# Optimization experiments

Hardware: AMD Instinct MI355X
Metric: run time of the kernel (lower is better)

The kernel has to match this reference:

```python
import jax, jax.numpy as jnp
import numpy as np
import math

DIM = 768
FFN_DIM = 4 * DIM
EPS = 1e-5

def layer_norm(x, gamma, beta):
    mu = jnp.mean(x, axis=-1, keepdims=True)
    var = jnp.var(x, axis=-1, keepdims=True)
    return (x - mu) * jax.lax.rsqrt(var + EPS) * gamma + beta

def setup_inputs() -> dict:
    key = jax.random.key(0)
    ks = jax.random.split(key, 8)
    b, n, d = 8, 2048, DIM
    s = 1.0 / math.sqrt(d)
    x = jax.random.normal(ks[0], (b, n, d), dtype=jnp.float32)
    Wq = jax.random.normal(ks[1], (d, d), dtype=jnp.float32) * s
    Wk = jax.random.normal(ks[2], (d, d), dtype=jnp.float32) * s
    Wv = jax.random.normal(ks[3], (d, d), dtype=jnp.float32) * s
    W1 = jax.random.normal(ks[4], (d, FFN_DIM), dtype=jnp.float32) * s
    b1 = jnp.zeros((FFN_DIM,), dtype=jnp.float32)
    W2 = jax.random.normal(ks[5], (FFN_DIM, d), dtype=jnp.float32) * (1.0 / math.sqrt(FFN_DIM))
    b2 = jnp.zeros((d,), dtype=jnp.float32)
    g1 = jnp.ones((d,), dtype=jnp.float32); be1 = jnp.zeros((d,), dtype=jnp.float32)
    g2 = jnp.ones((d,), dtype=jnp.float32); be2 = jnp.zeros((d,), dtype=jnp.float32)
    return {"x": x, "Wq": Wq, "Wk": Wk, "Wv": Wv, "ln1_g": g1, "ln1_b": be1,
            "W1": W1, "b1": b1, "W2": W2, "b2": b2, "ln2_g": g2, "ln2_b": be2}

def reference(x, Wq, Wk, Wv, ln1_g, ln1_b, W1, b1, W2, b2, ln2_g, ln2_b):
    # Self-attention (single head, full dim; dropout in eval mode => identity)
    Q = jnp.einsum('bnd,de->bne', x, Wq)
    K = jnp.einsum('bnd,de->bne', x, Wk)
    V = jnp.einsum('bnd,de->bne', x, Wv)
    scores = jnp.einsum('bnd,bmd->bnm', Q, K) / math.sqrt(DIM)  # [b,n,n]
    attn = jax.nn.softmax(scores, axis=-1)
    O = jnp.einsum('bnm,bmd->bnd', attn, V)
    h = layer_norm(x + O, ln1_g, ln1_b)
    # FFN with exact GELU (torch nn.GELU default)
    hidden = jax.nn.gelu(jnp.einsum('bnd,df->bnf', h, W1) + b1, approximate=False)
    out = jnp.einsum('bnf,fd->bnd', hidden, W2) + b2
    return layer_norm(h + out, ln2_g, ln2_b)
```

## Files before the change

### kernel.cpp

```cpp
#include <hip/hip_runtime.h>
#include <hip/hip_bf16.h>
#include <math.h>

using u16 = unsigned short;
typedef __bf16 bf16x8 __attribute__((ext_vector_type(8)));
typedef float f32x4 __attribute__((ext_vector_type(4)));
typedef u16 u16x8 __attribute__((ext_vector_type(8)));

__device__ __forceinline__ u16 f2b(float f) {
  union { float f; unsigned u; } c; c.f = f;
  unsigned r = c.u + 0x7fffu + ((c.u >> 16) & 1u);
  return (u16)(r >> 16);
}
__device__ __forceinline__ float b2f(u16 h) {
  union { unsigned u; float f; } c; c.u = ((unsigned)h) << 16;
  return c.f;
}

__device__ __forceinline__ float fast_gelu(float t) {
  float y = fminf(1.5957691216f * t + 0.07135481283f * t * t * t, 80.f);
  float e = __expf(y);
  return t * e * (1.0f / (e + 1.0f));
}

#define EPI_BF16 0
#define EPI_BF16_SCALE 1
#define EPI_GELU_BIAS 2
#define EPI_F32_BIAS 3
#define EPI_BF16_BIAS 4

#define GLDS16(src, dst)                                                     \
  __builtin_amdgcn_global_load_lds(                                          \
      (const __attribute__((address_space(1))) void*)(src),                  \
      (__attribute__((address_space(3))) void*)(dst), 16, 0, 0)

__device__ __forceinline__ int xswz(int o, int n) {
  int q = n >> 3, r = n & 7, x = o & 7, i = o >> 3;
  return (x < r ? x * (q + 1) : r * (q + 1) + (x - r) * q) + i;
}

template <int EPI>
__device__ __forceinline__ void epi_store(
    void* Cg, const float* bias, float v, long long off, int ccol, float scale)
{
  if (EPI == EPI_BF16) {
    ((u16*)Cg)[off] = f2b(v);
  } else if (EPI == EPI_BF16_SCALE) {
    ((u16*)Cg)[off] = f2b(v * scale);
  } else if (EPI == EPI_GELU_BIAS) {
    ((u16*)Cg)[off] = f2b(fast_gelu(v + bias[ccol]));
  } else if (EPI == EPI_F32_BIAS) {
    ((float*)Cg)[off] = v + bias[ccol];
  } else {
    ((u16*)Cg)[off] = f2b(v + bias[ccol]);
  }
}

template <int EPI>
__global__ __launch_bounds__(512, 2) void gemm256(
    const u16* __restrict__ Ag, const u16* __restrict__ Bg,
    void* __restrict__ Cg, const float* __restrict__ bias,
    int nbx, int K, float scale, int lda, int ldb, int ldc,
    long long sAz, long long sBz, long long sCz)
{
  __shared__ __align__(16) u16 lds[65536];

  const int tid = threadIdx.x;
  const int wave = tid >> 6, lane = tid & 63;
  const int wr = wave >> 2, wc = wave & 3;
  const int id = xswz(blockIdx.x, gridDim.x);
  const int bx = id % nbx, by = id / nbx;
  const int m0 = by * 256, n0 = bx * 256;
  const long long z = blockIdx.z;
  const u16* A = Ag + z * sAz + (long long)m0 * lda;
  const u16* B = Bg + z * sBz + (long long)n0 * ldb;

  const int rA = wave * 32 + (lane >> 2);
  const int slot = (lane & 3) ^ ((rA >> 1) & 3);
  const u16* a0 = A + (long long)rA * lda + slot * 8;
  const u16* a1 = a0 + (long long)16 * lda;
  const u16* b0 = B + (long long)rA * ldb + slot * 8;
  const u16* b1 = b0 + (long long)16 * ldb;
  const int d0 = wave * 32 * 32;
  const int d1 = (wave * 32 + 16) * 32;

  int offA[8], offB[4];
#pragma unroll
  for (int mf = 0; mf < 8; ++mf) {
    int r = wr * 128 + mf * 16 + (lane & 15);
    int b = r * 64 + ((lane >> 4) << 4);
    offA[mf] = b ^ (((b >> 7) & 3) << 4);
  }
#pragma unroll
  for (int nf = 0; nf < 4; ++nf) {
    int r = wc * 64 + nf * 16 + (lane & 15);
    int b = r * 64 + ((lane >> 4) << 4);
    offB[nf] = b ^ (((b >> 7) & 3) << 4);
  }

  f32x4 acc[8][4];
#pragma unroll
  for (int m = 0; m < 8; ++m)
#pragma unroll
    for (int n = 0; n < 4; ++n) acc[m][n] = f32x4{0.f, 0.f, 0.f, 0.f};

  const char* ldsc = (const char*)lds;
  const int NT = K >> 6;

  GLDS16(a0, lds + 0 * 8192 + d0);  GLDS16(a1, lds + 0 * 8192 + d1);
  GLDS16(b0, lds + 2 * 8192 + d0);  GLDS16(b1, lds + 2 * 8192 + d1);
  GLDS16(a0 + 32, lds + 1 * 8192 + d0);  GLDS16(a1 + 32, lds + 1 * 8192 + d1);
  GLDS16(b0 + 32, lds + 3 * 8192 + d0);  GLDS16(b1 + 32, lds + 3 * 8192 + d1);
  asm volatile("s_waitcnt vmcnt(4)" ::: "memory");
  asm volatile("s_barrier" ::: "memory");

  for (int t = 0; t < NT; ++t) {
    const int buf = t & 1, nb = buf ^ 1;
    const int kc = (t + 1 < NT) ? ((t + 1) << 6) : 0;
    const char* pA0 = ldsc + (buf * 4 + 0) * 16384;
    const char* pA1 = ldsc + (buf * 4 + 1) * 16384;
    const char* pB0 = ldsc + (buf * 4 + 2) * 16384;
    const char* pB1 = ldsc + (buf * 4 + 3) * 16384;
    u16* q = lds + nb * 4 * 8192;

    bf16x8 Af[4], Bf[4];

    GLDS16(a0 + kc, q + 0 * 8192 + d0);  GLDS16(a1 + kc, q + 0 * 8192 + d1);
    GLDS16(b0 + kc, q + 2 * 8192 + d0);  GLDS16(b1 + kc, q + 2 * 8192 + d1);
#pragma unroll
    for (int m = 0; m < 4; ++m) Af[m] = *(const bf16x8*)(pA0 + offA[m]);
#pragma unroll
    for (int n = 0; n < 4; ++n) Bf[n] = *(const bf16x8*)(pB0 + offB[n]);
    __builtin_amdgcn_s_setprio(1);
#pragma unroll
    for (int m = 0; m < 4; ++m)
#pragma unroll
      for (int n = 0; n < 4; ++n)
        acc[m][n] = __builtin_amdgcn_mfma_f32_16x16x32_bf16(Af[m], Bf[n], acc[m][n], 0, 0, 0);
    __builtin_amdgcn_s_setprio(0);

    GLDS16(a0 + kc + 32, q + 1 * 8192 + d0);  GLDS16(a1 + kc + 32, q + 1 * 8192 + d1);
    GLDS16(b0 + kc + 32, q + 3 * 8192 + d0);  GLDS16(b1 + kc + 32, q + 3 * 8192 + d1);
#pragma unroll
    for (int m = 0; m < 4; ++m) Af[m] = *(const bf16x8*)(pA0 + offA[4 + m]);
    __builtin_amdgcn_s_setprio(1);
#pragma unroll
    for (int m = 0; m < 4; ++m)
#pragma unroll
      for (int n = 0; n < 4; ++n)
        acc[4 + m][n] = __builtin_amdgcn_mfma_f32_16x16x32_bf16(Af[m], Bf[n], acc[4 + m][n], 0, 0, 0);
    __builtin_amdgcn_s_setprio(0);
    asm volatile("s_waitcnt vmcnt(8)" ::: "memory");
    asm volatile("s_barrier" ::: "memory");

#pragma unroll
    for (int m = 0; m < 4; ++m) Af[m] = *(const bf16x8*)(pA1 + offA[m]);
#pragma unroll
    for (int n = 0; n < 4; ++n) Bf[n] = *(const bf16x8*)(pB1 + offB[n]);
    __builtin_amdgcn_s_setprio(1);
#pragma unroll
    for (int m = 0; m < 4; ++m)
#pragma unroll
      for (int n = 0; n < 4; ++n)
        acc[m][n] = __builtin_amdgcn_mfma_f32_16x16x32_bf16(Af[m], Bf[n], acc[m][n], 0, 0, 0);
    __builtin_amdgcn_s_setprio(0);

#pragma unroll
    for (int m = 0; m < 4; ++m) Af[m] = *(const bf16x8*)(pA1 + offA[4 + m]);
    __builtin_amdgcn_s_setprio(1);
#pragma unroll
    for (int m = 0; m < 4; ++m)
#pragma unroll
      for (int n = 0; n < 4; ++n)
        acc[4 + m][n] = __builtin_amdgcn_mfma_f32_16x16x32_bf16(Af[m], Bf[n], acc[4 + m][n], 0, 0, 0);
    __builtin_amdgcn_s_setprio(0);
    asm volatile("s_waitcnt vmcnt(4)" ::: "memory");
    asm volatile("s_barrier" ::: "memory");
  }

#pragma unroll
  for (int mf = 0; mf < 8; ++mf) {
#pragma unroll
    for (int nf = 0; nf < 4; ++nf) {
      const int crow = m0 + wr * 128 + mf * 16 + (lane >> 4) * 4;
      const int ccol = n0 + wc * 64 + nf * 16 + (lane & 15);
#pragma unroll
      for (int j = 0; j < 4; ++j) {
        const long long off = (long long)(crow + j) * ldc + ccol + z * sCz;
        epi_store<EPI>(Cg, bias, acc[mf][nf][j], off, ccol, scale);
      }
    }
  }
}

template <int EPI>
__global__ __launch_bounds__(256, 2) void gemm128(
    const u16* __restrict__ Ag, const u16* __restrict__ Bg,
    void* __restrict__ Cg, const float* __restrict__ bias,
    int nbx, int K, float scale, int lda, int ldb, int ldc,
    long long sAz, long long sBz, long long sCz)
{
  __shared__ __align__(16) u16 lds[32768];

  const int tid = threadIdx.x;
  const int wave = tid >> 6, lane = tid & 63;
  const int wr = wave >> 1, wc = wave & 1;
  const int id = xswz(blockIdx.x, gridDim.x);
  const int bx = id % nbx, by = id / nbx;
  const int m0 = by * 128, n0 = bx * 128;
  const long long z = blockIdx.z;
  const u16* A = Ag + z * sAz + (long long)m0 * lda;
  const u16* B = Bg + z * sBz + (long long)n0 * ldb;

  const int rA = wave * 32 + (lane >> 2);
  const int slot = (lane & 3) ^ ((rA >> 1) & 3);
  const u16* a0 = A + (long long)rA * lda + slot * 8;
  const u16* a1 = a0 + (long long)16 * lda;
  const u16* b0 = B + (long long)rA * ldb + slot * 8;
  const u16* b1 = b0 + (long long)16 * ldb;
  const int d0 = wave * 32 * 32;
  const int d1 = (wave * 32 + 16) * 32;

  int offA[4], offB[4];
#pragma unroll
  for (int f = 0; f < 4; ++f) {
    int ra = wr * 64 + f * 16 + (lane & 15);
    int ba = ra * 64 + ((lane >> 4) << 4);
    offA[f] = ba ^ (((ba >> 7) & 3) << 4);
    int rb = wc * 64 + f * 16 + (lane & 15);
    int bb = rb * 64 + ((lane >> 4) << 4);
    offB[f] = bb ^ (((bb >> 7) & 3) << 4);
  }

  f32x4 acc[4][4];
#pragma unroll
  for (int m = 0; m < 4; ++m)
#pragma unroll
    for (int n = 0; n < 4; ++n) acc[m][n] = f32x4{0.f, 0.f, 0.f, 0.f};

  const char* ldsc = (const char*)lds;
  const int NT = K >> 6;

  GLDS16(a0, lds + 0 * 4096 + d0);  GLDS16(a1, lds + 0 * 4096 + d1);
  GLDS16(b0, lds + 2 * 4096 + d0);  GLDS16(b1, lds + 2 * 4096 + d1);
  GLDS16(a0 + 32, lds + 1 * 4096 + d0);  GLDS16(a1 + 32, lds + 1 * 4096 + d1);
  GLDS16(b0 + 32, lds + 3 * 4096 + d0);  GLDS16(b1 + 32, lds + 3 * 4096 + d1);
  asm volatile("s_waitcnt vmcnt(4)" ::: "memory");
  asm volatile("s_barrier" ::: "memory");

  for (int t = 0; t < NT; ++t) {
    const int buf = t & 1, nb = buf ^ 1;
    const int kc = (t + 1 < NT) ? ((t + 1) << 6) : 0;
    const char* pA0 = ldsc + (buf * 4 + 0) * 8192;
    const char* pA1 = ldsc + (buf * 4 + 1) * 8192;
    const char* pB0 = ldsc + (buf * 4 + 2) * 8192;
    const char* pB1 = ldsc + (buf * 4 + 3) * 8192;
    u16* q = lds + nb * 4 * 4096;

    bf16x8 Af[4], Bf[4];

    GLDS16(a0 + kc, q + 0 * 4096 + d0);  GLDS16(a1 + kc, q + 0 * 4096 + d1);
    GLDS16(b0 + kc, q + 2 * 4096 + d0);  GLDS16(b1 + kc, q + 2 * 4096 + d1);
#pragma unroll
    for (int m = 0; m < 4; ++m) Af[m] = *(const bf16x8*)(pA0 + offA[m]);
#pragma unroll
    for (int n = 0; n < 4; ++n) Bf[n] = *(const bf16x8*)(pB0 + offB[n]);
    __builtin_amdgcn_s_setprio(1);
#pragma unroll
    for (int m = 0; m < 4; ++m)
#pragma unroll
      for (int n = 0; n < 4; ++n)
        acc[m][n] = __builtin_amdgcn_mfma_f32_16x16x32_bf16(Af[m], Bf[n], acc[m][n], 0, 0, 0);
    __builtin_amdgcn_s_setprio(0);
    asm volatile("s_waitcnt vmcnt(4)" ::: "memory");
    asm volatile("s_barrier" ::: "memory");

    GLDS16(a0 + kc + 32, q + 1 * 4096 + d0);  GLDS16(a1 + kc + 32, q + 1 * 4096 + d1);
    GLDS16(b0 + kc + 32, q + 3 * 4096 + d0);  GLDS16(b1 + kc + 32, q + 3 * 4096 + d1);
#pragma unroll
    for (int m = 0; m < 4; ++m) Af[m] = *(const bf16x8*)(pA1 + offA[m]);
#pragma unroll
    for (int n = 0; n < 4; ++n) Bf[n] = *(const bf16x8*)(pB1 + offB[n]);
    __builtin_amdgcn_s_setprio(1);
#pragma unroll
    for (int m = 0; m < 4; ++m)
#pragma unroll
      for (int n = 0; n < 4; ++n)
        acc[m][n] = __builtin_amdgcn_mfma_f32_16x16x32_bf16(Af[m], Bf[n], acc[m][n], 0, 0, 0);
    __builtin_amdgcn_s_setprio(0);
    asm volatile("s_waitcnt vmcnt(4)" ::: "memory");
    asm volatile("s_barrier" ::: "memory");
  }

#pragma unroll
  for (int mf = 0; mf < 4; ++mf) {
#pragma unroll
    for (int nf = 0; nf < 4; ++nf) {
      const int crow = m0 + wr * 64 + mf * 16 + (lane >> 4) * 4;
      const int ccol = n0 + wc * 64 + nf * 16 + (lane & 15);
#pragma unroll
      for (int j = 0; j < 4; ++j) {
        const long long off = (long long)(crow + j) * ldc + ccol + z * sCz;
        epi_store<EPI>(Cg, bias, acc[mf][nf][j], off, ccol, scale);
      }
    }
  }
}

__global__ __launch_bounds__(256) void cast_f32_bf16(
    const float* __restrict__ x, u16* __restrict__ y, long long n4)
{
  const long long i = (long long)blockIdx.x * 256 + threadIdx.x;
  if (i >= n4) return;
  const float4 v = ((const float4*)x)[i];
  ushort4 o;
  o.x = f2b(v.x); o.y = f2b(v.y); o.z = f2b(v.z); o.w = f2b(v.w);
  ((ushort4*)y)[i] = o;
}

template <bool SRC_BF16>
__global__ __launch_bounds__(256) void transpose_cast(
    const void* __restrict__ srcv, u16* __restrict__ dst, int R, int C, int ldsrc,
    long long szSrc, long long szDst)
{
  __shared__ float tile[32][33];
  const long long zs = (long long)blockIdx.z * szSrc;
  const long long zd = (long long)blockIdx.z * szDst;
  const int c0 = blockIdx.x * 32, r0 = blockIdx.y * 32;
  const int tx = threadIdx.x & 31, ty = threadIdx.x >> 5;
#pragma unroll
  for (int i = 0; i < 4; ++i) {
    const int r = r0 + ty + i * 8;
    float v;
    if (SRC_BF16) v = b2f(((const u16*)srcv)[zs + (long long)r * ldsrc + c0 + tx]);
    else          v = ((const float*)srcv)[zs + (long long)r * ldsrc + c0 + tx];
    tile[ty + i * 8][tx] = v;
  }
  __syncthreads();
#pragma unroll
  for (int i = 0; i < 4; ++i) {
    const int c = c0 + ty + i * 8;
    dst[zd + (long long)c * R + r0 + tx] = f2b(tile[tx][ty + i * 8]);
  }
}

__global__ __launch_bounds__(256) void softmax_rows(
    u16* __restrict__ S, int ncol)
{
  __shared__ float red[8];
  const long long row = blockIdx.x;
  u16* s = S + row * ncol;
  const int t = threadIdx.x;

  const u16x8 u = *(const u16x8*)&s[t * 8];
  float v[8];
#pragma unroll
  for (int j = 0; j < 8; ++j) v[j] = b2f(u[j]);

  float mx = v[0];
#pragma unroll
  for (int j = 1; j < 8; ++j) mx = fmaxf(mx, v[j]);
  for (int o = 32; o; o >>= 1) mx = fmaxf(mx, __shfl_xor(mx, o));
  if ((t & 63) == 0) red[t >> 6] = mx;
  __syncthreads();
  mx = fmaxf(fmaxf(red[0], red[1]), fmaxf(red[2], red[3]));

  float sum = 0.f;
#pragma unroll
  for (int j = 0; j < 8; ++j) { v[j] = __expf(v[j] - mx); sum += v[j]; }
  for (int o = 32; o; o >>= 1) sum += __shfl_xor(sum, o);
  if ((t & 63) == 0) red[4 + (t >> 6)] = sum;
  __syncthreads();
  sum = red[4] + red[5] + red[6] + red[7];

  const float inv = 1.0f / sum;
  u16x8 o8;
#pragma unroll
  for (int j = 0; j < 8; ++j) o8[j] = f2b(v[j] * inv);
  *(u16x8*)&s[t * 8] = o8;
}

__global__ __launch_bounds__(256) void ln1_kernel(
    const float* __restrict__ x, const u16* __restrict__ O,
    const float* __restrict__ g, const float* __restrict__ be,
    u16* __restrict__ h)
{
  __shared__ float red[8];
  const long long row = blockIdx.x;
  const float* xr = x + row * 768;
  const u16* orow = O + row * 768;
  const int t = threadIdx.x, base = t * 3;

  float v[3];
#pragma unroll
  for (int j = 0; j < 3; ++j) v[j] = xr[base + j] + b2f(orow[base + j]);
  float s = v[0] + v[1] + v[2];
  float ss = v[0] * v[0] + v[1] * v[1] + v[2] * v[2];
  for (int o = 32; o; o >>= 1) { s += __shfl_xor(s, o); ss += __shfl_xor(ss, o); }
  if ((t & 63) == 0) { red[t >> 6] = s; red[4 + (t >> 6)] = ss; }
  __syncthreads();
  s = red[0] + red[1] + red[2] + red[3];
  ss = red[4] + red[5] + red[6] + red[7];
  const float mu = s * (1.0f / 768.0f);
  const float var = ss * (1.0f / 768.0f) - mu * mu;
  const float inv = rsqrtf(var + 1e-5f);
#pragma unroll
  for (int j = 0; j < 3; ++j) {
    const float o = (v[j] - mu) * inv * g[base + j] + be[base + j];
    h[row * 768 + base + j] = f2b(o);
  }
}

__global__ __launch_bounds__(256) void ln2_kernel(
    const u16* __restrict__ h, const u16* __restrict__ ob,
    const float* __restrict__ g, const float* __restrict__ be,
    float* __restrict__ y)
{
  __shared__ float red[8];
  const long long row = blockIdx.x;
  const u16* hr = h + row * 768;
  const u16* orow = ob + row * 768;
  const int t = threadIdx.x, base = t * 3;

  float v[3];
#pragma unroll
  for (int j = 0; j < 3; ++j) v[j] = b2f(hr[base + j]) + b2f(orow[base + j]);
  float s = v[0] + v[1] + v[2];
  float ss = v[0] * v[0] + v[1] * v[1] + v[2] * v[2];
  for (int o = 32; o; o >>= 1) { s += __shfl_xor(s, o); ss += __shfl_xor(ss, o); }
  if ((t & 63) == 0) { red[t >> 6] = s; red[4 + (t >> 6)] = ss; }
  __syncthreads();
  s = red[0] + red[1] + red[2] + red[3];
  ss = red[4] + red[5] + red[6] + red[7];
  const float mu = s * (1.0f / 768.0f);
  const float var = ss * (1.0f / 768.0f) - mu * mu;
  const float inv = rsqrtf(var + 1e-5f);
#pragma unroll
  for (int j = 0; j < 3; ++j) {
    y[row * 768 + base + j] = (v[j] - mu) * inv * g[base + j] + be[base + j];
  }
}

extern "C" void kernel_launch(void* const* d_in, const int* in_sizes, int n_in,
                              void* d_out, int out_size, void* d_ws, size_t ws_size,
                              hipStream_t stream)
{
  const int Bb = 8, Nn = 2048, D = 768, F = 3072, E = 1536;
  const int M = Bb * Nn;
  const long long MD = (long long)M * D;

  const float* x   = (const float*)d_in[0];
  const float* Wq  = (const float*)d_in[1];
  const float* Wk  = (const float*)d_in[2];
  const float* Wv  = (const float*)d_in[3];
  const float* g1  = (const float*)d_in[4];
  const float* be1 = (const float*)d_in[5];
  const float* W1  = (const float*)d_in[6];
  const float* b1  = (const float*)d_in[7];
  const float* W2  = (const float*)d_in[8];
  const float* b2  = (const float*)d_in[9];
  const float* g2  = (const float*)d_in[10];
  const float* be2 = (const float*)d_in[11];

  u16* xb   = (u16*)d_out;
  u16* wqkt = xb + MD;
  u16* wvt  = wqkt + (size_t)E * D;

  char* w = (char*)d_ws;
  size_t off = 0;
  auto alloc = [&](size_t bytes) { void* p = w + off; off += bytes; return p; };
  u16* w1t = (u16*)alloc((size_t)F * D * 2);
  u16* w2t = (u16*)alloc((size_t)D * F * 2);
  u16* hb  = (u16*)alloc((size_t)MD * 2);
  u16* qk  = (u16*)alloc((size_t)M * E * 2);
  u16* Vt  = (u16*)alloc((size_t)Bb * D * Nn * 2);
  u16* S   = (u16*)alloc((size_t)Bb * Nn * Nn * 2);
  u16* O   = (u16*)alloc((size_t)MD * 2);
  u16* hidden = qk;
  u16* outf   = qk + (size_t)M * F;

  const dim3 tcb(256);
  const float scl = 0.03608439182435161f;

  cast_f32_bf16<<<(unsigned)(MD / 4 / 256), 256, 0, stream>>>(x, xb, MD / 4);
  transpose_cast<false><<<dim3(D / 32, D / 32, 1), tcb, 0, stream>>>(Wq, wqkt, D, D, D, 0, 0);
  transpose_cast<false><<<dim3(D / 32, D / 32, 1), tcb, 0, stream>>>(Wk, wqkt + D * D, D, D, D, 0, 0);
  transpose_cast<false><<<dim3(D / 32, D / 32, 1), tcb, 0, stream>>>(Wv, wvt, D, D, D, 0, 0);
  transpose_cast<false><<<dim3(F / 32, D / 32, 1), tcb, 0, stream>>>(W1, w1t, D, F, F, 0, 0);
  transpose_cast<false><<<dim3(D / 32, F / 32, 1), tcb, 0, stream>>>(W2, w2t, F, D, D, 0, 0);

  gemm256<EPI_BF16><<<dim3(6 * 64, 1, 1), 512, 0, stream>>>(
      xb, wqkt, qk, nullptr, 6, D, 1.f, D, D, E, 0, 0, 0);

  gemm128<EPI_BF16><<<dim3(16 * 6, 1, Bb), 256, 0, stream>>>(
      wvt, xb, Vt, nullptr, 16, D, 1.f, D, D, Nn,
      0, (long long)Nn * D, (long long)D * Nn);

  gemm256<EPI_BF16_SCALE><<<dim3(8 * 8, 1, Bb), 512, 0, stream>>>(
      qk, qk + D, S, nullptr, 8, D, scl, E, E, Nn,
      (long long)Nn * E, (long long)Nn * E, (long long)Nn * Nn);

  softmax_rows<<<M, 256, 0, stream>>>(S, Nn);

  gemm128<EPI_BF16><<<dim3(6 * 16, 1, Bb), 256, 0, stream>>>(
      S, Vt, O, nullptr, 6, Nn, 1.f, Nn, Nn, D,
      (long long)Nn * Nn, (long long)D * Nn, (long long)Nn * D);

  ln1_kernel<<<M, 256, 0, stream>>>(x, O, g1, be1, hb);

  gemm256<EPI_GELU_BIAS><<<dim3(12 * 64, 1, 1), 512, 0, stream>>>(
      hb, w1t, hidden, b1, 12, D, 1.f, D, D, F, 0, 0, 0);

  gemm128<EPI_BF16_BIAS><<<dim3(6 * 128, 1, 1), 256, 0, stream>>>(
      hidden, w2t, outf, b2, 6, F, 1.f, F, F, D, 0, 0, 0);

  ln2_kernel<<<M, 256, 0, stream>>>(hb, outf, g2, be2, (float*)d_out);
}
```

Baseline: 501.1 us.

## Fuse softmax exp and row-sum into QK^T GEMM epilogue, defer normalization to LN1

Removes the separate softmax kernel. The QK^T GEMM epilogue now writes exp(score) without subtracting the row max, clamped at 60, and atomically accumulates per-row sums into a zeroed float buffer. LN1 divides the unnormalized PV output by that sum. This saves a full read and write pass over the large score matrix, at the cost of skipping max subtraction (overflow or precision risk for large scores), atomics, and an extra zeroing kernel. The gemm256 main loop is also reordered to interleave the A and B tile loads with extra barriers, and gemm128 gets extra barriers too.

After: 488.2 us. 1.03x faster.

```diff
diff --git a/kernel.cpp b/kernel.cpp
--- a/kernel.cpp
+++ b/kernel.cpp
@@ -24,9 +24,8 @@
 }
 
 #define EPI_BF16 0
-#define EPI_BF16_SCALE 1
+#define EPI_EXP_SUM 1
 #define EPI_GELU_BIAS 2
-#define EPI_F32_BIAS 3
 #define EPI_BF16_BIAS 4
 
 #define GLDS16(src, dst)                                                     \
@@ -45,12 +44,8 @@
 {
   if (EPI == EPI_BF16) {
     ((u16*)Cg)[off] = f2b(v);
-  } else if (EPI == EPI_BF16_SCALE) {
-    ((u16*)Cg)[off] = f2b(v * scale);
   } else if (EPI == EPI_GELU_BIAS) {
     ((u16*)Cg)[off] = f2b(fast_gelu(v + bias[ccol]));
-  } else if (EPI == EPI_F32_BIAS) {
-    ((float*)Cg)[off] = v + bias[ccol];
   } else {
     ((u16*)Cg)[off] = f2b(v + bias[ccol]);
   }
@@ -61,7 +56,8 @@
     const u16* __restrict__ Ag, const u16* __restrict__ Bg,
     void* __restrict__ Cg, const float* __restrict__ bias,
     int nbx, int K, float scale, int lda, int ldb, int ldc,
-    long long sAz, long long sBz, long long sCz)
+    long long sAz, long long sBz, long long sCz,
+    float* __restrict__ lsum, int lzs)
 {
   __shared__ __align__(16) u16 lds[65536];
 
@@ -125,12 +121,13 @@
 
     bf16x8 Af[4], Bf[4];
 
-    GLDS16(a0 + kc, q + 0 * 8192 + d0);  GLDS16(a1 + kc, q + 0 * 8192 + d1);
-    GLDS16(b0 + kc, q + 2 * 8192 + d0);  GLDS16(b1 + kc, q + 2 * 8192 + d1);
+    GLDS16(a0 + kc, q + 0 * 8192 + d0);
+    GLDS16(a1 + kc, q + 0 * 8192 + d1);
 #pragma unroll
     for (int m = 0; m < 4; ++m) Af[m] = *(const bf16x8*)(pA0 + offA[m]);
 #pragma unroll
     for (int n = 0; n < 4; ++n) Bf[n] = *(const bf16x8*)(pB0 + offB[n]);
+    asm volatile("s_barrier" ::: "memory");
     __builtin_amdgcn_s_setprio(1);
 #pragma unroll
     for (int m = 0; m < 4; ++m)
@@ -138,35 +135,13 @@
       for (int n = 0; n < 4; ++n)
         acc[m][n] = __builtin_amdgcn_mfma_f32_16x16x32_bf16(Af[m], Bf[n], acc[m][n], 0, 0, 0);
     __builtin_amdgcn_s_setprio(0);
-
-    GLDS16(a0 + kc + 32, q + 1 * 8192 + d0);  GLDS16(a1 + kc + 32, q + 1 * 8192 + d1);
-    GLDS16(b0 + kc + 32, q + 3 * 8192 + d0);  GLDS16(b1 + kc + 32, q + 3 * 8192 + d1);
+    asm volatile("s_barrier" ::: "memory");
+
+    GLDS16(b0 + kc, q + 2 * 8192 + d0);
+    GLDS16(b1 + kc, q + 2 * 8192 + d1);
 #pragma unroll
     for (int m = 0; m < 4; ++m) Af[m] = *(const bf16x8*)(pA0 + offA[4 + m]);
-    __builtin_amdgcn_s_setprio(1);
-#pragma unroll
-    for (int m = 0; m < 4; ++m)
-#pragma unroll
-      for (int n = 0; n < 4; ++n)
-        acc[4 + m][n] = __builtin_amdgcn_mfma_f32_16x16x32_bf16(Af[m], Bf[n], acc[4 + m][n], 0, 0, 0);
-    __builtin_amdgcn_s_setprio(0);
-    asm volatile("s_waitcnt vmcnt(8)" ::: "memory");
-    asm volatile("s_barrier" ::: "memory");
-
-#pragma unroll
-    for (int m = 0; m < 4; ++m) Af[m] = *(const bf16x8*)(pA1 + offA[m]);
-#pragma unroll
-    for (int n = 0; n < 4; ++n) Bf[n] = *(const bf16x8*)(pB1 + offB[n]);
-    __builtin_amdgcn_s_setprio(1);
-#pragma unroll
-    for (int m = 0; m < 4; ++m)
-#pragma unroll
-      for (int n = 0; n < 4; ++n)
-        acc[m][n] = __builtin_amdgcn_mfma_f32_16x16x32_bf16(Af[m], Bf[n], acc[m][n], 0, 0, 0);
-    __builtin_amdgcn_s_setprio(0);
-
-#pragma unroll
-    for (int m = 0; m < 4; ++m) Af[m] = *(const bf16x8*)(pA1 + offA[4 + m]);
+    asm volatile("s_barrier" ::: "memory");
     __builtin_amdgcn_s_setprio(1);
 #pragma unroll
     for (int m = 0; m < 4; ++m)
@@ -176,18 +151,76 @@
     __builtin_amdgcn_s_setprio(0);
     asm volatile("s_waitcnt vmcnt(4)" ::: "memory");
     asm volatile("s_barrier" ::: "memory");
-  }
-
-#pragma unroll
-  for (int mf = 0; mf < 8; ++mf) {
-#pragma unroll
-    for (int nf = 0; nf < 4; ++nf) {
+
+    GLDS16(a0 + kc + 32, q + 1 * 8192 + d0);
+    GLDS16(a1 + kc + 32, q + 1 * 8192 + d1);
+#pragma unroll
+    for (int m = 0; m < 4; ++m) Af[m] = *(const bf16x8*)(pA1 + offA[m]);
+#pragma unroll
+    for (int n = 0; n < 4; ++n) Bf[n] = *(const bf16x8*)(pB1 + offB[n]);
+    asm volatile("s_barrier" ::: "memory");
+    __builtin_amdgcn_s_setprio(1);
+#pragma unroll
+    for (int m = 0; m < 4; ++m)
+#pragma unroll
+      for (int n = 0; n < 4; ++n)
+        acc[m][n] = __builtin_amdgcn_mfma_f32_16x16x32_bf16(Af[m], Bf[n], acc[m][n], 0, 0, 0);
+    __builtin_amdgcn_s_setprio(0);
+    asm volatile("s_barrier" ::: "memory");
+
+    GLDS16(b0 + kc + 32, q + 3 * 8192 + d0);
+    GLDS16(b1 + kc + 32, q + 3 * 8192 + d1);
+#pragma unroll
+    for (int m = 0; m < 4; ++m) Af[m] = *(const bf16x8*)(pA1 + offA[4 + m]);
+    asm volatile("s_barrier" ::: "memory");
+    __builtin_amdgcn_s_setprio(1);
+#pragma unroll
+    for (int m = 0; m < 4; ++m)
+#pragma unroll
+      for (int n = 0; n < 4; ++n)
+        acc[4 + m][n] = __builtin_amdgcn_mfma_f32_16x16x32_bf16(Af[m], Bf[n], acc[4 + m][n], 0, 0, 0);
+    __builtin_amdgcn_s_setprio(0);
+    asm volatile("s_waitcnt vmcnt(4)" ::: "memory");
+    asm volatile("s_barrier" ::: "memory");
+  }
+
+  if (EPI == EPI_EXP_SUM) {
+#pragma unroll
+    for (int mf = 0; mf < 8; ++mf) {
       const int crow = m0 + wr * 128 + mf * 16 + (lane >> 4) * 4;
-      const int ccol = n0 + wc * 64 + nf * 16 + (lane & 15);
+      float part[4] = {0.f, 0.f, 0.f, 0.f};
+#pragma unroll
+      for (int nf = 0; nf < 4; ++nf) {
+        const int ccol = n0 + wc * 64 + nf * 16 + (lane & 15);
+#pragma unroll
+        for (int j = 0; j < 4; ++j) {
+          const float p = __expf(fminf(acc[mf][nf][j] * scale, 60.f));
+          const u16 ub = f2b(p);
+          ((u16*)Cg)[(long long)(crow + j) * ldc + ccol + z * sCz] = ub;
+          part[j] += b2f(ub);
+        }
+      }
 #pragma unroll
       for (int j = 0; j < 4; ++j) {
-        const long long off = (long long)(crow + j) * ldc + ccol + z * sCz;
-        epi_store<EPI>(Cg, bias, acc[mf][nf][j], off, ccol, scale);
+        float s = part[j];
+        s += __shfl_xor(s, 1); s += __shfl_xor(s, 2);
+        s += __shfl_xor(s, 4); s += __shfl_xor(s, 8);
+        if ((lane & 15) == 0)
+          atomicAdd(&lsum[(long long)z * lzs + crow + j], s);
+      }
+    }
+  } else {
+#pragma unroll
+    for (int mf = 0; mf < 8; ++mf) {
+#pragma unroll
+      for (int nf = 0; nf < 4; ++nf) {
+        const int crow = m0 + wr * 128 + mf * 16 + (lane >> 4) * 4;
+        const int ccol = n0 + wc * 64 + nf * 16 + (lane & 15);
+#pragma unroll
+        for (int j = 0; j < 4; ++j) {
+          const long long off = (long long)(crow + j) * ldc + ccol + z * sCz;
+          epi_store<EPI>(Cg, bias, acc[mf][nf][j], off, ccol, scale);
+        }
       }
     }
   }
@@ -265,6 +298,7 @@
     for (int m = 0; m < 4; ++m) Af[m] = *(const bf16x8*)(pA0 + offA[m]);
 #pragma unroll
     for (int n = 0; n < 4; ++n) Bf[n] = *(const bf16x8*)(pB0 + offB[n]);
+    asm volatile("s_barrier" ::: "memory");
     __builtin_amdgcn_s_setprio(1);
 #pragma unroll
     for (int m = 0; m < 4; ++m)
@@ -281,6 +315,7 @@
     for (int m = 0; m < 4; ++m) Af[m] = *(const bf16x8*)(pA1 + offA[m]);
 #pragma unroll
     for (int n = 0; n < 4; ++n) Bf[n] = *(const bf16x8*)(pB1 + offB[n]);
+    asm volatile("s_barrier" ::: "memory");
     __builtin_amdgcn_s_setprio(1);
 #pragma unroll
     for (int m = 0; m < 4; ++m)
@@ -305,6 +340,11 @@
       }
     }
   }
+}
+
+__global__ __launch_bounds__(256) void zero_f32(float* __restrict__ p, int n) {
+  const int i = blockIdx.x * 256 + threadIdx.x;
+  if (i < n) p[i] = 0.f;
 }
 
 __global__ __launch_bounds__(256) void cast_f32_bf16(
@@ -344,44 +384,9 @@
   }
 }
 
-__global__ __launch_bounds__(256) void softmax_rows(
-    u16* __restrict__ S, int ncol)
-{
-  __shared__ float red[8];
-  const long long row = blockIdx.x;
-  u16* s = S + row * ncol;
-  const int t = threadIdx.x;
-
-  const u16x8 u = *(const u16x8*)&s[t * 8];
-  float v[8];
-#pragma unroll
-  for (int j = 0; j < 8; ++j) v[j] = b2f(u[j]);
-
-  float mx = v[0];
-#pragma unroll
-  for (int j = 1; j < 8; ++j) mx = fmaxf(mx, v[j]);
-  for (int o = 32; o; o >>= 1) mx = fmaxf(mx, __shfl_xor(mx, o));
-  if ((t & 63) == 0) red[t >> 6] = mx;
-  __syncthreads();
-  mx = fmaxf(fmaxf(red[0], red[1]), fmaxf(red[2], red[3]));
-
-  float sum = 0.f;
-#pragma unroll
-  for (int j = 0; j < 8; ++j) { v[j] = __expf(v[j] - mx); sum += v[j]; }
-  for (int o = 32; o; o >>= 1) sum += __shfl_xor(sum, o);
-  if ((t & 63) == 0) red[4 + (t >> 6)] = sum;
-  __syncthreads();
-  sum = red[4] + red[5] + red[6] + red[7];
-
-  const float inv = 1.0f / sum;
-  u16x8 o8;
-#pragma unroll
-  for (int j = 0; j < 8; ++j) o8[j] = f2b(v[j] * inv);
-  *(u16x8*)&s[t * 8] = o8;
-}
-
 __global__ __launch_bounds__(256) void ln1_kernel(
     const float* __restrict__ x, const u16* __restrict__ O,
+    const float* __restrict__ l,
     const float* __restrict__ g, const float* __restrict__ be,
     u16* __restrict__ h)
 {
@@ -389,11 +394,12 @@
   const long long row = blockIdx.x;
   const float* xr = x + row * 768;
   const u16* orow = O + row * 768;
+  const float invl = 1.0f / l[row];
   const int t = threadIdx.x, base = t * 3;
 
   float v[3];
 #pragma unroll
-  for (int j = 0; j < 3; ++j) v[j] = xr[base + j] + b2f(orow[base + j]);
+  for (int j = 0; j < 3; ++j) v[j] = xr[base + j] + b2f(orow[base + j]) * invl;
   float s = v[0] + v[1] + v[2];
   float ss = v[0] * v[0] + v[1] * v[1] + v[2] * v[2];
   for (int o = 32; o; o >>= 1) { s += __shfl_xor(s, o); ss += __shfl_xor(ss, o); }
@@ -472,6 +478,7 @@
   u16* w1t = (u16*)alloc((size_t)F * D * 2);
   u16* w2t = (u16*)alloc((size_t)D * F * 2);
   u16* hb  = (u16*)alloc((size_t)MD * 2);
+  float* lrow = (float*)alloc((size_t)M * 4);
   u16* qk  = (u16*)alloc((size_t)M * E * 2);
   u16* Vt  = (u16*)alloc((size_t)Bb * D * Nn * 2);
   u16* S   = (u16*)alloc((size_t)Bb * Nn * Nn * 2);
@@ -482,6 +489,7 @@
   const dim3 tcb(256);
   const float scl = 0.03608439182435161f;
 
+  zero_f32<<<M / 256, 256, 0, stream>>>(lrow, M);
   cast_f32_bf16<<<(unsigned)(MD / 4 / 256), 256, 0, stream>>>(x, xb, MD / 4);
   transpose_cast<false><<<dim3(D / 32, D / 32, 1), tcb, 0, stream>>>(Wq, wqkt, D, D, D, 0, 0);
   transpose_cast<false><<<dim3(D / 32, D / 32, 1), tcb, 0, stream>>>(Wk, wqkt + D * D, D, D, D, 0, 0);
@@ -490,26 +498,24 @@
   transpose_cast<false><<<dim3(D / 32, F / 32, 1), tcb, 0, stream>>>(W2, w2t, F, D, D, 0, 0);
 
   gemm256<EPI_BF16><<<dim3(6 * 64, 1, 1), 512, 0, stream>>>(
-      xb, wqkt, qk, nullptr, 6, D, 1.f, D, D, E, 0, 0, 0);
+      xb, wqkt, qk, nullptr, 6, D, 1.f, D, D, E, 0, 0, 0, nullptr, 0);
 
   gemm128<EPI_BF16><<<dim3(16 * 6, 1, Bb), 256, 0, stream>>>(
       wvt, xb, Vt, nullptr, 16, D, 1.f, D, D, Nn,
       0, (long long)Nn * D, (long long)D * Nn);
 
-  gemm256<EPI_BF16_SCALE><<<dim3(8 * 8, 1, Bb), 512, 0, stream>>>(
+  gemm256<EPI_EXP_SUM><<<dim3(8 * 8, 1, Bb), 512, 0, stream>>>(
       qk, qk + D, S, nullptr, 8, D, scl, E, E, Nn,
-      (long long)Nn * E, (long long)Nn * E, (long long)Nn * Nn);
-
-  softmax_rows<<<M, 256, 0, stream>>>(S, Nn);
+      (long long)Nn * E, (long long)Nn * E, (long long)Nn * Nn, lrow, Nn);
 
   gemm128<EPI_BF16><<<dim3(6 * 16, 1, Bb), 256, 0, stream>>>(
       S, Vt, O, nullptr, 6, Nn, 1.f, Nn, Nn, D,
       (long long)Nn * Nn, (long long)D * Nn, (long long)Nn * D);
 
-  ln1_kernel<<<M, 256, 0, stream>>>(x, O, g1, be1, hb);
+  ln1_kernel<<<M, 256, 0, stream>>>(x, O, lrow, g1, be1, hb);
 
   gemm256<EPI_GELU_BIAS><<<dim3(12 * 64, 1, 1), 512, 0, stream>>>(
-      hb, w1t, hidden, b1, 12, D, 1.f, D, D, F, 0, 0, 0);
+      hb, w1t, hidden, b1, 12, D, 1.f, D, D, F, 0, 0, 0, nullptr, 0);
 
   gemm128<EPI_BF16_BIAS><<<dim3(6 * 128, 1, 1), 256, 0, stream>>>(
       hidden, w2t, outf, b2, 6, F, 1.f, F, F, D, 0, 0, 0);
```
